# Performance work log

Hardware: AMD Instinct MI355X
Metric: run time of the kernel (lower is better)

Reference implementation:

```python
import jax, jax.numpy as jnp
import numpy as np

B, T, D, H = 8, 2048, 512, 2048
EPS = 1e-5


def setup_inputs() -> dict:
    key = jax.random.key(0)
    ks = jax.random.split(key, 12)
    s_d = 1.0 / np.sqrt(D)
    s_h = 1.0 / np.sqrt(H)
    s_w = np.sqrt(6.0 / (T + T))  # xavier_uniform scale for w [T,T]
    return {
        "x": jax.random.normal(ks[0], (B, T, D), jnp.float32),
        "ln1_g": jnp.ones((D,), jnp.float32),
        "ln1_b": jnp.zeros((D,), jnp.float32),
        "Wk": jax.random.normal(ks[1], (D, D), jnp.float32) * s_d,
        "bk": jnp.zeros((D,), jnp.float32),
        "Wv": jax.random.normal(ks[2], (D, D), jnp.float32) * s_d,
        "bv": jnp.zeros((D,), jnp.float32),
        "Wq": jax.random.normal(ks[3], (D, D), jnp.float32) * s_d,
        "bq": jnp.zeros((D,), jnp.float32),
        "w": jax.random.uniform(ks[4], (T, T), jnp.float32, -s_w, s_w),
        "Wo": jax.random.normal(ks[5], (D, D), jnp.float32) * s_d,
        "bo": jnp.zeros((D,), jnp.float32),
        "ln2_g": jnp.ones((D,), jnp.float32),
        "ln2_b": jnp.zeros((D,), jnp.float32),
        "W1": jax.random.normal(ks[6], (D, H), jnp.float32) * s_d,
        "b1": jnp.zeros((H,), jnp.float32),
        "W2": jax.random.normal(ks[7], (H, D), jnp.float32) * s_h,
        "b2": jnp.zeros((D,), jnp.float32),
    }


def _ln(x, g, b):
    mu = jnp.mean(x, axis=-1, keepdims=True)
    var = jnp.mean(jnp.square(x - mu), axis=-1, keepdims=True)
    return (x - mu) * jax.lax.rsqrt(var + EPS) * g + b


def _aft_full(h, Wk, bk, Wv, bv, Wq, bq, w, Wo, bo):
    # h: [B,T,D]
    K = h @ Wk + bk
    V = h @ Wv + bv
    # row-max stabilized position bias [T,T]
    exp_w = jnp.exp(w - jnp.max(w, axis=-1, keepdims=True))
    # NOTE: original stabilizes K with max over dim=0 (the BATCH dim) -- faithful
    exp_K = jnp.exp(K - jnp.max(K, axis=0, keepdims=True))  # [B,T,D]
    num = jnp.einsum("ts,bsd->btd", exp_w, exp_K * V)
    den = jnp.einsum("ts,bsd->btd", exp_w, exp_K)
    Yt = num / den
    Q = h @ Wq + bq
    Yt = jax.nn.sigmoid(Q) * Yt
    return Yt @ Wo + bo


def reference(x, ln1_g, ln1_b, Wk, bk, Wv, bv, Wq, bq, w, Wo, bo,
              ln2_g, ln2_b, W1, b1, W2, b2):
    attn = _aft_full(_ln(x, ln1_g, ln1_b), Wk, bk, Wv, bv, Wq, bq, w, Wo, bo)
    out = attn + x
    h = _ln(out, ln2_g, ln2_b)
    h = jax.nn.gelu(h @ W1 + b1, approximate=False)
    h = jax.nn.gelu(h @ W2 + b2, approximate=False)  # GELU after 2nd linear too (faithful)
    return h + out
```

## Files before the change

### kernel.cpp

```cpp
#include <hip/hip_runtime.h>
#include <hip/hip_bf16.h>
#include <math.h>

typedef __hip_bfloat16 bf16;
typedef __bf16 bf16x8 __attribute__((ext_vector_type(8)));
typedef float f32x4 __attribute__((ext_vector_type(4)));

#define B_ 8
#define T_ 2048
#define D_ 512
#define H_ 2048

__device__ __forceinline__ float b2f(unsigned short u) {
    return __uint_as_float((unsigned)u << 16);
}
__device__ __forceinline__ float ldf(const float* p, long i) { return p[i]; }
__device__ __forceinline__ float ldf(const bf16* p, long i) {
    return b2f(((const unsigned short*)p)[i]);
}
__device__ __forceinline__ float gelu_f(float v) {
    float a = 1.5957691216057308f * (v + 0.044715f * v * v * v);
    return v / (1.0f + __expf(-a));
}

__device__ __forceinline__ long poff(int row, int col, int K) {
    return ((long)(row >> 4) * (K >> 5) + (col >> 5)) * 512 + (row & 15) * 32 + (col & 31);
}

#define GLD16(g, l)                                                          \
    __builtin_amdgcn_global_load_lds(                                        \
        (const __attribute__((address_space(1))) void*)(g),                  \
        (__attribute__((address_space(3))) void*)(l), 16, 0, 0)

template <typename Tin, bool PACKO>
__device__ __forceinline__ void ln_body(const Tin* __restrict__ x,
                                        const float* __restrict__ g,
                                        const float* __restrict__ bb,
                                        bf16* __restrict__ y, int row, int tid,
                                        float* red) {
    long base = (long)row * D_;
    float v0 = ldf(x, base + tid);
    float v1 = ldf(x, base + tid + 256);
    float s = v0 + v1;
#pragma unroll
    for (int off = 32; off > 0; off >>= 1) s += __shfl_down(s, off);
    int lane = tid & 63, wid = tid >> 6;
    if (lane == 0) red[wid] = s;
    __syncthreads();
    float mean = (red[0] + red[1] + red[2] + red[3]) * (1.0f / 512.0f);
    __syncthreads();
    float d0 = v0 - mean, d1 = v1 - mean;
    float vs = d0 * d0 + d1 * d1;
#pragma unroll
    for (int off = 32; off > 0; off >>= 1) vs += __shfl_down(vs, off);
    if (lane == 0) red[wid] = vs;
    __syncthreads();
    float var = (red[0] + red[1] + red[2] + red[3]) * (1.0f / 512.0f);
    float rstd = rsqrtf(var + 1e-5f);
    float o0 = d0 * rstd * g[tid] + bb[tid];
    float o1 = d1 * rstd * g[tid + 256] + bb[tid + 256];
    if (PACKO) {
        y[poff(row, tid, D_)]       = __float2bfloat16(o0);
        y[poff(row, tid + 256, D_)] = __float2bfloat16(o1);
    } else {
        y[base + tid]       = __float2bfloat16(o0);
        y[base + tid + 256] = __float2bfloat16(o1);
    }
}

template <typename Tin, bool PACKO>
__global__ __launch_bounds__(256) void ln_kernel(const Tin* __restrict__ x,
                                                 const float* __restrict__ g,
                                                 const float* __restrict__ bb,
                                                 bf16* __restrict__ y) {
    __shared__ float red[4];
    ln_body<Tin, PACKO>(x, g, bb, y, blockIdx.x, threadIdx.x, red);
}

struct WT6 {
    const float* src[6];
    bf16* dst[6];
    int K[6], N[6];
};

__global__ __launch_bounds__(256) void prep_kernel(WT6 p,
                                                   const float* __restrict__ x,
                                                   const float* __restrict__ ln1g,
                                                   const float* __restrict__ ln1b,
                                                   bf16* __restrict__ h1,
                                                   const float* __restrict__ w,
                                                   bf16* __restrict__ ew) {
    __shared__ float sbuf[64][65];
    int bid = blockIdx.x;
    int tid = threadIdx.x;
    if (bid < 6144) {
        int z = bid >> 10;
        int rem = bid & 1023;
        int n0 = (rem & 31) * 64, k0 = (rem >> 5) * 64;
        int K = p.K[z], N = p.N[z];
        if (n0 >= N || k0 >= K) return;
        const float* W = p.src[z];
        bf16* WT = p.dst[z];
        int tx = tid & 63, ty = tid >> 6;
#pragma unroll
        for (int r = 0; r < 16; ++r) {
            int kl = r * 4 + ty;
            sbuf[kl][tx] = W[(long)(k0 + kl) * N + n0 + tx];
        }
        __syncthreads();
#pragma unroll
        for (int r = 0; r < 16; ++r) {
            int nl = r * 4 + ty;
            WT[poff(n0 + nl, k0 + tx, K)] = __float2bfloat16(sbuf[tx][nl]);
        }
    } else if (bid < 6144 + 16384) {
        ln_body<float, true>(x, ln1g, ln1b, h1, bid - 6144, tid, &sbuf[0][0]);
    } else {
        int row = bid - (6144 + 16384);
        long base = (long)row * T_;
        float v[8];
        float mx = -3.4e38f;
#pragma unroll
        for (int i = 0; i < 8; ++i) {
            v[i] = w[base + tid + i * 256];
            mx = fmaxf(mx, v[i]);
        }
#pragma unroll
        for (int off = 32; off > 0; off >>= 1) mx = fmaxf(mx, __shfl_down(mx, off));
        float* red = &sbuf[0][0];
        if ((tid & 63) == 0) red[tid >> 6] = mx;
        __syncthreads();
        float rmax = fmaxf(fmaxf(red[0], red[1]), fmaxf(red[2], red[3]));
#pragma unroll
        for (int i = 0; i < 8; ++i)
            ew[poff(row, tid + i * 256, T_)] = __float2bfloat16(expf(v[i] - rmax));
    }
}

__global__ __launch_bounds__(256) void maxk_kernel(const bf16* __restrict__ K,
                                                   bf16* __restrict__ mk) {
    long i = (long)blockIdx.x * 256 + threadIdx.x;
    float m = ldf(K, i);
#pragma unroll
    for (int b = 1; b < B_; ++b) m = fmaxf(m, ldf(K, (long)b * (T_ * D_) + i));
    mk[i] = __float2bfloat16(m);
}

__global__ __launch_bounds__(256) void kv2t_kernel(const bf16* __restrict__ K_,
                                                   const bf16* __restrict__ V_,
                                                   const bf16* __restrict__ mk,
                                                   bf16* __restrict__ kv2t) {
    __shared__ float sev[64][65];
    __shared__ float se[64][65];
    int tx = threadIdx.x & 63, ty = threadIdx.x >> 6;
    int t0 = blockIdx.x * 64, d0 = blockIdx.y * 64, b = blockIdx.z;
    long ibase = (long)b << 20;
#pragma unroll
    for (int r = 0; r < 16; ++r) {
        int tl = r * 4 + ty;
        long mi = (long)(t0 + tl) * D_ + d0 + tx;
        float e = expf(ldf(K_, ibase + mi) - ldf(mk, mi));
        sev[tl][tx] = e * ldf(V_, ibase + mi);
        se[tl][tx] = e;
    }
    __syncthreads();
    long obase = (long)b << 21;
#pragma unroll
    for (int r = 0; r < 16; ++r) {
        int d = d0 + r * 4 + ty;
        int nrow = ((d >> 4) << 5) + (d & 15);
        kv2t[obase + poff(nrow,      t0 + tx, T_)] = __float2bfloat16(sev[tx][r * 4 + ty]);
        kv2t[obase + poff(nrow + 16, t0 + tx, T_)] = __float2bfloat16(se[tx][r * 4 + ty]);
    }
}

template <int BM, int PK>
__global__ __launch_bounds__(256, 4) void mfma_gemm(
    const bf16* __restrict__ A, const bf16* __restrict__ Bt,
    const float* __restrict__ b0, const float* __restrict__ b1,
    const float* __restrict__ b2,
    bf16* __restrict__ Cb, float* __restrict__ Cf,
    const bf16* __restrict__ resb, const float* __restrict__ resf,
    bf16* __restrict__ yq,
    int M, int N, int K, int modes, long bsB, long bsC, long planeStride) {
    constexpr int MI = BM / 32;
    constexpr int NA = BM / 64;
    constexpr int PL = (BM + 128) * 32;
    constexpr bool PA = PK & 1, PB = PK & 2, PCK = PK & 4;
    constexpr long astep = PA ? 512 : 32;
    constexpr long bstep = PB ? 512 : 32;
    __shared__ short Sh[2 * PL];
    int tid = threadIdx.x;
    int lane = tid & 63, wave = tid >> 6;
    int wm = wave & 1, wn = wave >> 1;

    int gx = gridDim.x, gy = gridDim.y;
    long nwg = (long)gx * gy * gridDim.z;
    long o = blockIdx.x + (long)gx * (blockIdx.y + (long)gy * blockIdx.z);
    long wk = (o & 7) * (nwg >> 3) + (o >> 3);
    int bx = (int)(wk % gx);
    long rq = wk / gx;
    int by = (int)(rq % gy);
    int bz = (int)(rq / gy);
    int m0 = by * BM, n0 = bx * 128;

    const short* Ag = (const short*)A;
    const short* Bg = (const short*)Bt + (long)bz * bsB;

    int lr = lane >> 2;
    int le = (lane & 3) * 8;
    const short* ga[NA];
    short* la[NA];
#pragma unroll
    for (int i = 0; i < NA; ++i) {
        int arow = m0 + wave * (BM / 4) + i * 16;
        ga[i] = PA ? Ag + (long)(arow >> 4) * ((long)K << 4) + lane * 8
                   : Ag + (long)(arow + lr) * K + le;
        la[i] = Sh + (wave * (BM / 4) + i * 16) * 32;
    }
    int brow = n0 + wave * 32;
    const short* gb0 = PB ? Bg + (long)(brow >> 4) * ((long)K << 4) + lane * 8
                          : Bg + (long)(brow + lr) * K + le;
    const short* gb1 = PB ? gb0 + ((long)K << 4) : gb0 + 16L * K;
    short* lb0 = Sh + BM * 32 + (wave * 32) * 32;
    short* lb1 = lb0 + 16 * 32;

    f32x4 acc[MI][4];
    f32x4 zz = {0.f, 0.f, 0.f, 0.f};
#pragma unroll
    for (int i = 0; i < MI; ++i)
#pragma unroll
        for (int j = 0; j < 4; ++j) acc[i][j] = zz;

    int fr = lane & 15;
    int fk = (lane >> 4) * 8;
    int rm = wm * (BM / 2);

    auto stage = [&](int kt, int ofs) {
#pragma unroll
        for (int i = 0; i < NA; ++i) GLD16(ga[i] + kt * astep, la[i] + ofs);
        GLD16(gb0 + kt * bstep, lb0 + ofs);
        GLD16(gb1 + kt * bstep, lb1 + ofs);
    };
    auto compute = [&](int ofs) {
        const short* Asb = Sh + ofs;
        const short* Bsb = Sh + ofs + BM * 32;
        bf16x8 af[MI], bv[4];
#pragma unroll
        for (int mi = 0; mi < MI; ++mi)
            af[mi] = *(const bf16x8*)(Asb + (rm + mi * 16 + fr) * 32 + fk);
#pragma unroll
        for (int ni = 0; ni < 4; ++ni)
            bv[ni] = *(const bf16x8*)(Bsb + (wn * 64 + ni * 16 + fr) * 32 + fk);
#pragma unroll
        for (int mi = 0; mi < MI; ++mi)
#pragma unroll
            for (int ni = 0; ni < 4; ++ni)
                acc[mi][ni] = __builtin_amdgcn_mfma_f32_16x16x32_bf16(
                    af[mi], bv[ni], acc[mi][ni], 0, 0, 0);
    };

    int nk = K >> 5;
    stage(0, 0);
    __syncthreads();
    for (int kt = 0; kt < nk; kt += 2) {
        if (kt + 1 < nk) stage(kt + 1, PL);
        compute(0);
        __syncthreads();
        if (kt + 2 < nk) stage(kt + 2, 0);
        compute(PL);
        __syncthreads();
    }

    int cc = lane & 15, cr = (lane >> 4) * 4;
    if (yq) {
        long qb = (long)bz * (long)(T_ * D_);
        int dbase = (n0 + wn * 64) >> 1;
#pragma unroll
        for (int mi = 0; mi < MI; ++mi) {
            int row0 = m0 + rm + mi * 16 + cr;
#pragma unroll
            for (int pp = 0; pp < 2; ++pp) {
                int d = dbase + pp * 16 + cc;
#pragma unroll
                for (int r = 0; r < 4; ++r) {
                    long qi = qb + (long)(row0 + r) * D_ + d;
                    float sq = ldf((const bf16*)yq, qi);
                    yq[qi] = __float2bfloat16(sq * acc[mi][2 * pp][r] /
                                              acc[mi][2 * pp + 1][r]);
                }
            }
        }
        return;
    }
    long cbase = (long)bz * bsC;
#pragma unroll
    for (int mi = 0; mi < MI; ++mi) {
#pragma unroll
        for (int ni = 0; ni < 4; ++ni) {
            int row0 = m0 + rm + mi * 16 + cr;
            int col = n0 + wn * 64 + ni * 16 + cc;
            float bvl;
            long colterm;
            int md, rowstride;
            if (planeStride) {
                int plane = col >> 9;
                int c2 = col & 511;
                const float* bp = (plane == 0) ? b0 : ((plane == 1) ? b1 : b2);
                bvl = bp[c2];
                md = (modes >> (2 * plane)) & 3;
                colterm = (long)plane * planeStride + c2;
                rowstride = 512;
            } else {
                bvl = b0 ? b0[col] : 0.0f;
                md = modes & 3;
                colterm = col;
                rowstride = N;
            }
#pragma unroll
            for (int r = 0; r < 4; ++r) {
                float v = acc[mi][ni][r] + bvl;
                if (md == 1) v = 1.0f / (1.0f + __expf(-v));
                else if (md == 2) v = gelu_f(v);
                long idx;
                if (PCK) idx = cbase + poff(row0 + r, col, N);
                else     idx = cbase + (long)(row0 + r) * rowstride + colterm;
                if (resf) v += resf[idx];
                if (resb) v += ldf(resb, idx);
                if (Cf) Cf[idx] = v;
                else Cb[idx] = __float2bfloat16(v);
            }
        }
    }
}

extern "C" void kernel_launch(void* const* d_in, const int* in_sizes, int n_in,
                              void* d_out, int out_size, void* d_ws, size_t ws_size,
                              hipStream_t stream) {
    const float* x    = (const float*)d_in[0];
    const float* ln1g = (const float*)d_in[1];
    const float* ln1b = (const float*)d_in[2];
    const float* Wk   = (const float*)d_in[3];
    const float* bk   = (const float*)d_in[4];
    const float* Wv   = (const float*)d_in[5];
    const float* bv   = (const float*)d_in[6];
    const float* Wq   = (const float*)d_in[7];
    const float* bq   = (const float*)d_in[8];
    const float* w    = (const float*)d_in[9];
    const float* Wo   = (const float*)d_in[10];
    const float* bo   = (const float*)d_in[11];
    const float* ln2g = (const float*)d_in[12];
    const float* ln2b = (const float*)d_in[13];
    const float* W1   = (const float*)d_in[14];
    const float* b1   = (const float*)d_in[15];
    const float* W2   = (const float*)d_in[16];
    const float* b2   = (const float*)d_in[17];
    float* out = (float*)d_out;

    const long S_BTD = (long)B_ * T_ * D_;
    const long S_TD  = (long)T_ * D_;
    const long S_TT  = (long)T_ * T_;
    const long S_B2D = (long)B_ * T_ * 2 * D_;
    const long S_DD  = (long)D_ * D_;

    bf16* h1     = (bf16*)d_ws;
    bf16* outres = h1 + S_BTD;
    bf16* ew     = outres + S_BTD;
    bf16* KVQ    = ew + S_TT;
    bf16* kv2t   = KVQ + 3 * S_BTD;
    bf16* mk     = kv2t + S_B2D;
    bf16* WkT    = mk + 2 * S_TD;
    bf16* WvT    = WkT + S_DD;
    bf16* WqT    = WvT + S_DD;
    bf16* WoT    = WqT + S_DD;
    bf16* W1T    = WoT + S_DD;
    bf16* W2T    = W1T + (long)D_ * H_;
    bf16* Kb  = KVQ;
    bf16* Vb  = KVQ + S_BTD;
    bf16* Qb  = KVQ + 2 * S_BTD;
    bf16* hH  = KVQ;
    bf16* h2  = h1;

    const int M = B_ * T_;

    WT6 p;
    p.src[0] = Wk; p.src[1] = Wv; p.src[2] = Wq; p.src[3] = Wo; p.src[4] = W1; p.src[5] = W2;
    p.dst[0] = WkT; p.dst[1] = WvT; p.dst[2] = WqT; p.dst[3] = WoT; p.dst[4] = W1T; p.dst[5] = W2T;
    p.K[0] = p.K[1] = p.K[2] = p.K[3] = 512; p.K[4] = 512; p.K[5] = 2048;
    p.N[0] = p.N[1] = p.N[2] = p.N[3] = 512; p.N[4] = 2048; p.N[5] = 512;

    prep_kernel<<<6144 + 16384 + 2048, 256, 0, stream>>>(p, x, ln1g, ln1b, h1, w, ew);
    mfma_gemm<128, 3><<<dim3(1536 / 128, M / 128, 1), 256, 0, stream>>>(
        h1, WkT, bk, bv, bq, Kb, nullptr, nullptr, nullptr, nullptr,
        M, 1536, D_, (1 << 4), 0, 0, S_BTD);
    maxk_kernel<<<S_TD / 256, 256, 0, stream>>>(Kb, mk);
    kv2t_kernel<<<dim3(T_ / 64, D_ / 64, B_), 256, 0, stream>>>(Kb, Vb, mk, kv2t);
    mfma_gemm<128, 3><<<dim3(1024 / 128, T_ / 128, B_), 256, 0, stream>>>(
        ew, kv2t, nullptr, nullptr, nullptr, nullptr, nullptr, nullptr, nullptr, Qb,
        T_, 1024, T_, 0, (long)1024 * T_, 0, 0);
    mfma_gemm<128, 2><<<dim3(D_ / 128, M / 128, 1), 256, 0, stream>>>(
        Qb, WoT, bo, nullptr, nullptr, outres, nullptr, nullptr, x, nullptr,
        M, D_, D_, 0, 0, 0, 0);
    ln_kernel<bf16, true><<<M, 256, 0, stream>>>(outres, ln2g, ln2b, h2);
    mfma_gemm<128, 7><<<dim3(H_ / 128, M / 128, 1), 256, 0, stream>>>(
        h2, W1T, b1, nullptr, nullptr, hH, nullptr, nullptr, nullptr, nullptr,
        M, H_, D_, 2, 0, 0, 0);
    mfma_gemm<128, 3><<<dim3(D_ / 128, M / 128, 1), 256, 0, stream>>>(
        hH, W2T, b2, nullptr, nullptr, nullptr, out, outres, nullptr, nullptr,
        M, D_, H_, 2, 0, 0, 0);
}
```

Baseline: 445.6 us.

## Add 256x256 eight-wave MFMA GEMM for AFT mixing and FFN up-projection

Adds a new GEMM kernel with 256x256 tiles, 512 threads (8 waves), direct global-to-LDS loads, double-buffered LDS and a phased schedule using barriers, waitcnt gating and setprio around the MFMA bursts. It also remaps workgroup IDs across groups of eight. It replaces the 128-tile GEMM for the exp_w x (expK*V, expK) mixing step, with the num/den divide and sigmoid(Q) gating fused into the epilogue, and for the W1+GELU projection. The larger tiles are meant to raise data reuse per LDS byte and to overlap loads with compute. The cost is heavy register and LDS use (128KB shared) and fewer workgroups.

```diff
diff --git a/kernel.cpp b/kernel.cpp
--- a/kernel.cpp
+++ b/kernel.cpp
@@ -31,6 +31,12 @@
     __builtin_amdgcn_global_load_lds(                                        \
         (const __attribute__((address_space(1))) void*)(g),                  \
         (__attribute__((address_space(3))) void*)(l), 16, 0, 0)
+
+__device__ __forceinline__ unsigned lds_off(const void* p) {
+    return (unsigned)(unsigned long long)(const __attribute__((address_space(3))) char*)p;
+}
+#define DSR(dst, a, OFF)                                                     \
+    asm volatile("ds_read_b128 %0, %1 offset:" #OFF : "=v"(dst) : "v"(a))
 
 template <typename Tin, bool PACKO>
 __device__ __forceinline__ void ln_body(const Tin* __restrict__ x,
@@ -329,6 +335,165 @@
                 if (resb) v += ldf(resb, idx);
                 if (Cf) Cf[idx] = v;
                 else Cb[idx] = __float2bfloat16(v);
+            }
+        }
+    }
+}
+
+#define PH_BAR  __builtin_amdgcn_s_barrier()
+#define PH_LGKM do { asm volatile("s_waitcnt lgkmcnt(0)" ::: "memory");      \
+                     __builtin_amdgcn_sched_barrier(0); } while (0)
+#define GATE4   asm volatile("s_waitcnt vmcnt(4)" ::: "memory")
+#define MMA4(MH)                                                             \
+    do {                                                                     \
+        __builtin_amdgcn_s_setprio(1);                                       \
+        _Pragma("unroll") for (int j = 0; j < 4; ++j) {                      \
+            _Pragma("unroll") for (int ni = 0; ni < 4; ++ni)                 \
+                acc[(MH) * 4 + j][ni] =                                      \
+                    __builtin_amdgcn_mfma_f32_16x16x32_bf16(                 \
+                        af[j], bv[ni], acc[(MH) * 4 + j][ni], 0, 0, 0);      \
+        }                                                                    \
+        __builtin_amdgcn_s_setprio(0);                                       \
+    } while (0)
+
+template <int EPI>
+__global__ __launch_bounds__(512, 2) void mfma_gemm8(
+    const bf16* __restrict__ A, const bf16* __restrict__ Bt,
+    const float* __restrict__ b0, bf16* __restrict__ Cb, bf16* __restrict__ yq,
+    int M, int N, int K, long bsB) {
+    __shared__ short Sh[65536];
+    int tid = threadIdx.x;
+    int lane = tid & 63, w = tid >> 6;
+    int wm = w >> 2, wn = w & 3;
+    int fr = lane & 15, fk = (lane >> 4) * 8;
+
+    int gx = gridDim.x, gy = gridDim.y;
+    long nwg = (long)gx * gy * gridDim.z;
+    long o = blockIdx.x + (long)gx * (blockIdx.y + (long)gy * blockIdx.z);
+    long wk = (o & 7) * (nwg >> 3) + (o >> 3);
+    int bx = (int)(wk % gx);
+    long rq = wk / gx;
+    int by = (int)(rq % gy);
+    int bz = (int)(rq / gy);
+    int m0 = by * 256, n0 = bx * 256;
+
+    const short* Ag = (const short*)A;
+    const short* Bg = (const short*)Bt + (long)bz * bsB;
+    int kt32 = K >> 5;
+
+    const short* sA0 = Ag + (long)((m0 >> 4) + 2 * w) * kt32 * 512 + lane * 8;
+    const short* sA1 = sA0 + (long)kt32 * 512;
+    const short* sB0 = Bg + (long)((n0 >> 4) + 2 * w) * kt32 * 512 + lane * 8;
+    const short* sB1 = sB0 + (long)kt32 * 512;
+    short* dA0 = Sh + ((2 * w) >> 3) * 8192 + ((2 * w) & 7) * 1024;
+    short* dA1 = Sh + ((2 * w + 1) >> 3) * 8192 + ((2 * w + 1) & 7) * 1024;
+    short* dB0 = dA0 + 16384;
+    short* dB1 = dA1 + 16384;
+    auto stageA = [&](int t, int kk) {
+        long so = (long)(t * 2 + kk) * 512;
+        int dof = (t & 1) * 32768 + kk * 512;
+        GLD16(sA0 + so, dA0 + dof);
+        GLD16(sA1 + so, dA1 + dof);
+    };
+    auto stageB = [&](int t, int kk) {
+        long so = (long)(t * 2 + kk) * 512;
+        int dof = (t & 1) * 32768 + kk * 512;
+        GLD16(sB0 + so, dB0 + dof);
+        GLD16(sB1 + so, dB1 + dof);
+    };
+
+    unsigned aBase = lds_off(Sh) + wm * 16384 + fr * 64 + fk * 2;
+    unsigned bBase = lds_off(Sh) + 32768 + (wn >> 1) * 16384 + (wn & 1) * 8192 +
+                     fr * 64 + fk * 2;
+    unsigned aB00 = aBase, aB01 = aBase + 1024, aB10 = aBase + 65536, aB11 = aBase + 66560;
+    unsigned bB00 = bBase, bB01 = bBase + 1024, bB10 = bBase + 65536, bB11 = bBase + 66560;
+
+    f32x4 acc[8][4];
+    f32x4 zz = {0.f, 0.f, 0.f, 0.f};
+#pragma unroll
+    for (int i = 0; i < 8; ++i)
+#pragma unroll
+        for (int j = 0; j < 4; ++j) acc[i][j] = zz;
+    bf16x8 af[4], bv[4];
+
+    auto rdA_lo = [&](unsigned b) {
+        DSR(af[0], b, 0); DSR(af[1], b, 2048); DSR(af[2], b, 4096); DSR(af[3], b, 6144);
+    };
+    auto rdA_hi = [&](unsigned b) {
+        DSR(af[0], b, 8192); DSR(af[1], b, 10240); DSR(af[2], b, 12288); DSR(af[3], b, 14336);
+    };
+    auto rdB = [&](unsigned b) {
+        DSR(bv[0], b, 0); DSR(bv[1], b, 2048); DSR(bv[2], b, 4096); DSR(bv[3], b, 6144);
+    };
+
+    stageA(0, 0); stageB(0, 0); stageA(0, 1); stageB(0, 1);
+    asm volatile("s_waitcnt vmcnt(4)" ::: "memory");
+    PH_BAR;
+
+    int nkt = K >> 6;
+    int niter = nkt >> 1;
+#pragma unroll 1
+    for (int i = 0; i < niter; ++i) {
+        int t1 = 2 * i + 1, t2 = 2 * i + 2;
+        bool st2 = t2 < nkt;
+        rdB(bB00); rdA_lo(aB00);
+        stageA(t1, 0);
+        PH_BAR; PH_LGKM; MMA4(0); PH_BAR;
+        rdA_hi(aB00);
+        stageB(t1, 0);
+        PH_BAR; PH_LGKM; MMA4(1); GATE4; PH_BAR;
+        rdB(bB01); rdA_lo(aB01);
+        stageA(t1, 1);
+        PH_BAR; PH_LGKM; MMA4(0); PH_BAR;
+        rdA_hi(aB01);
+        stageB(t1, 1);
+        PH_BAR; PH_LGKM; MMA4(1); GATE4; PH_BAR;
+        rdB(bB10); rdA_lo(aB10);
+        if (st2) stageA(t2, 0);
+        PH_BAR; PH_LGKM; MMA4(0); PH_BAR;
+        rdA_hi(aB10);
+        if (st2) stageB(t2, 0);
+        PH_BAR; PH_LGKM; MMA4(1); GATE4; PH_BAR;
+        rdB(bB11); rdA_lo(aB11);
+        if (st2) stageA(t2, 1);
+        PH_BAR; PH_LGKM; MMA4(0); PH_BAR;
+        rdA_hi(aB11);
+        if (st2) stageB(t2, 1);
+        PH_BAR; PH_LGKM; MMA4(1); GATE4; PH_BAR;
+    }
+
+    int cc = lane & 15, cr = (lane >> 4) * 4;
+    if (EPI == 1) {
+        long qb = (long)bz * (long)(T_ * D_);
+        int dbase = (n0 + wn * 64) >> 1;
+#pragma unroll
+        for (int mi = 0; mi < 8; ++mi) {
+            int row0 = m0 + wm * 128 + mi * 16 + cr;
+#pragma unroll
+            for (int pp = 0; pp < 2; ++pp) {
+                int d = dbase + pp * 16 + cc;
+#pragma unroll
+                for (int r = 0; r < 4; ++r) {
+                    long qi = qb + (long)(row0 + r) * D_ + d;
+                    float sq = ldf((const bf16*)yq, qi);
+                    yq[qi] = __float2bfloat16(sq * acc[mi][2 * pp][r] /
+                                              acc[mi][2 * pp + 1][r]);
+                }
+            }
+        }
+    } else {
+#pragma unroll
+        for (int mi = 0; mi < 8; ++mi) {
+            int row0 = m0 + wm * 128 + mi * 16 + cr;
+#pragma unroll
+            for (int ni = 0; ni < 4; ++ni) {
+                int col = n0 + wn * 64 + ni * 16 + cc;
+                float bvl = b0[col];
+#pragma unroll
+                for (int r = 0; r < 4; ++r) {
+                    float v = gelu_f(acc[mi][ni][r] + bvl);
+                    Cb[poff(row0 + r, col, N)] = __float2bfloat16(v);
+                }
             }
         }
     }
@@ -395,16 +560,14 @@
         M, 1536, D_, (1 << 4), 0, 0, S_BTD);
     maxk_kernel<<<S_TD / 256, 256, 0, stream>>>(Kb, mk);
     kv2t_kernel<<<dim3(T_ / 64, D_ / 64, B_), 256, 0, stream>>>(Kb, Vb, mk, kv2t);
-    mfma_gemm<128, 3><<<dim3(1024 / 128, T_ / 128, B_), 256, 0, stream>>>(
-        ew, kv2t, nullptr, nullptr, nullptr, nullptr, nullptr, nullptr, nullptr, Qb,
-        T_, 1024, T_, 0, (long)1024 * T_, 0, 0);
+    mfma_gemm8<1><<<dim3(1024 / 256, T_ / 256, B_), 512, 0, stream>>>(
+        ew, kv2t, nullptr, nullptr, Qb, T_, 1024, T_, (long)1024 * T_);
     mfma_gemm<128, 2><<<dim3(D_ / 128, M / 128, 1), 256, 0, stream>>>(
         Qb, WoT, bo, nullptr, nullptr, outres, nullptr, nullptr, x, nullptr,
         M, D_, D_, 0, 0, 0, 0);
     ln_kernel<bf16, true><<<M, 256, 0, stream>>>(outres, ln2g, ln2b, h2);
-    mfma_gemm<128, 7><<<dim3(H_ / 128, M / 128, 1), 256, 0, stream>>>(
-        h2, W1T, b1, nullptr, nullptr, hH, nullptr, nullptr, nullptr, nullptr,
-        M, H_, D_, 2, 0, 0, 0);
+    mfma_gemm8<0><<<dim3(H_ / 256, M / 256, 1), 512, 0, stream>>>(
+        h2, W1T, b1, hH, nullptr, M, H_, D_, 0);
     mfma_gemm<128, 3><<<dim3(D_ / 128, M / 128, 1), 256, 0, stream>>>(
         hH, W2T, b2, nullptr, nullptr, nullptr, out, outres, nullptr, nullptr,
         M, D_, H_, 2, 0, 0, 0);
```

After: 463.6 us. +4.0%, slower.
